# Kernel tuning notes

Hardware: AMD Instinct MI355X
Metric: run time of the kernel (lower is better)

## Reference

```python
import jax, jax.numpy as jnp
import numpy as np

WIRES = 4
NUM_LAYERS = 2


def setup_inputs() -> dict:
    key = jax.random.key(0)
    k1, k2 = jax.random.split(key)
    x = jax.random.uniform(k1, (8192, 1, 28, 28), dtype=jnp.float32)
    params = jax.random.normal(k2, (NUM_LAYERS, WIRES), dtype=jnp.float32)
    return {"x": x, "params": params}


def _apply_ry(state, theta, wire):
    # state: (B, P, 2,2,2,2) real (RY/CNOT circuit keeps amplitudes real)
    s = jnp.moveaxis(state, 2 + wire, -1)
    a, b = s[..., 0], s[..., 1]
    theta = jnp.asarray(theta)
    theta = theta.reshape(theta.shape + (1,) * (a.ndim - theta.ndim))
    c, sn = jnp.cos(theta / 2), jnp.sin(theta / 2)
    s = jnp.stack([c * a - sn * b, sn * a + c * b], axis=-1)
    return jnp.moveaxis(s, -1, 2 + wire)


def _cnot(state, ctrl, tgt):
    s = jnp.moveaxis(state, (2 + ctrl, 2 + tgt), (-2, -1))
    s = jnp.stack([s[..., 0, :], s[..., 1, ::-1]], axis=-2)
    return jnp.moveaxis(s, (-2, -1), (2 + ctrl, 2 + tgt))


def reference(x, params):
    B = x.shape[0]
    # 2x2 patches, row-major over (r, c); each flattened as [x00, x01, x10, x11]
    patches = x[:, 0].reshape(B, 14, 2, 14, 2).transpose(0, 1, 3, 2, 4).reshape(B, 196, 4)
    # |0000> for every (batch, patch)
    state = jnp.zeros((B, 196, 2, 2, 2, 2), dtype=x.dtype).at[:, :, 0, 0, 0, 0].set(1.0)
    # data-encoding RYs + entangling CNOT chain
    for w in range(WIRES):
        state = _apply_ry(state, patches[..., w], w)
    for w in range(WIRES - 1):
        state = _cnot(state, w, w + 1)
    # variational layers
    for layer in range(params.shape[0]):
        for w in range(WIRES):
            state = _apply_ry(state, params[layer, w], w)
        for w in range(WIRES - 1):
            state = _cnot(state, w, w + 1)
    # <Z_w> = P(bit_w = 0) - P(bit_w = 1)
    probs = state * state
    zs = []
    for w in range(WIRES):
        p = jnp.moveaxis(probs, 2 + w, 2)
        zs.append(p[:, :, 0].sum(axis=(2, 3, 4)) - p[:, :, 1].sum(axis=(2, 3, 4)))
    z = jnp.stack(zs, axis=-1)  # (B, 196, 4): 4 expvals per patch, patch-major
    return z.reshape(B, 196 * WIRES)
```

## Files before the change

kernel.cpp:

```cpp
#include <hip/hip_runtime.h>


typedef float f32x2 __attribute__((ext_vector_type(2)));

__device__ __forceinline__ f32x2 pk_fma(f32x2 a, f32x2 b, f32x2 c) {
    return __builtin_elementwise_fma(a, b, c);
}
__device__ __forceinline__ f32x2 splat(float v) { return (f32x2){v, v}; }
__device__ __forceinline__ float uniformf(float v) {
    return __int_as_float(__builtin_amdgcn_readfirstlane(__float_as_int(v)));
}

__device__ __forceinline__ void pk_sincos_half(f32x2 x, f32x2& s, f32x2& c) {
    f32x2 t = x * 0.5f;
    f32x2 u = t * t;
    f32x2 ps = pk_fma(u, splat(8.3333333e-3f), splat(-0.16666667f));
    ps = pk_fma(u, ps, splat(1.0f));
    s = t * ps;
    f32x2 pc = pk_fma(u, splat(-1.3888889e-3f), splat(4.1666667e-2f));
    pc = pk_fma(u, pc, splat(-0.5f));
    c = pk_fma(u, pc, splat(1.0f));
}

template <int W>
__device__ __forceinline__ void apply_ry_t(f32x2 st[16], f32x2 tb, f32x2 ntb) {
    constexpr int S = 8 >> W;
#pragma unroll
    for (int i = 0; i < 16; ++i) {
        if ((i & S) == 0) {
            f32x2 a = st[i], b = st[i | S];
            st[i]     = pk_fma(ntb, b, a);
            st[i | S] = pk_fma(tb, a, b);
        }
    }
}

template <int C, int T>
__device__ __forceinline__ void cnot(f32x2 st[16]) {
    constexpr int CS = 8 >> C, TS = 8 >> T;
#pragma unroll
    for (int i = 0; i < 16; ++i) {
        if ((i & CS) != 0 && (i & TS) == 0) {
            f32x2 t = st[i];
            st[i] = st[i | TS];
            st[i | TS] = t;
        }
    }
}

__global__ __launch_bounds__(256, 4) void quanv_kernel(
    const float* __restrict__ x,
    const float* __restrict__ params,
    float* __restrict__ out,
    int totalPairs)
{
    __shared__ float tl[8];
    int tid = threadIdx.x;
    if (tid < 8) tl[tid] = tanf(0.5f * params[tid]);

    int i = blockIdx.x * 256 + tid;
    int b  = i / 98;
    int q  = i - b * 98;
    int r  = q / 7;
    int cp = q - r * 7;
    bool valid = (i < totalPairs);

    const float* base = x + (size_t)b * 784 + r * 56 + cp * 4;
    float4 top = make_float4(0.f, 0.f, 0.f, 0.f), bot = top;
    if (valid) {
        top = *reinterpret_cast<const float4*>(base);
        bot = *reinterpret_cast<const float4*>(base + 28);
    }

    __syncthreads();
    float t0 = uniformf(tl[0]), t1 = uniformf(tl[1]);
    float t2 = uniformf(tl[2]), t3 = uniformf(tl[3]);
    float t4 = uniformf(tl[4]), t5 = uniformf(tl[5]);
    float t6 = uniformf(tl[6]), t7 = uniformf(tl[7]);
    if (!valid) return;

    f32x2 cw[4], sw[4];
    pk_sincos_half((f32x2){top.x, top.z}, sw[0], cw[0]);
    pk_sincos_half((f32x2){top.y, top.w}, sw[1], cw[1]);
    pk_sincos_half((f32x2){bot.x, bot.z}, sw[2], cw[2]);
    pk_sincos_half((f32x2){bot.y, bot.w}, sw[3], cw[3]);

    f32x2 st[16];
    {
        f32x2 r00 = cw[0] * cw[1], r01 = cw[0] * sw[1];
        f32x2 r10 = sw[0] * cw[1], r11 = sw[0] * sw[1];
        f32x2 q00 = cw[2] * cw[3], q01 = cw[2] * sw[3];
        f32x2 q10 = sw[2] * cw[3], q11 = sw[2] * sw[3];
        st[0]  = r00 * q00; st[1]  = r00 * q01; st[2]  = r00 * q10; st[3]  = r00 * q11;
        st[4]  = r01 * q00; st[5]  = r01 * q01; st[6]  = r01 * q10; st[7]  = r01 * q11;
        st[8]  = r10 * q00; st[9]  = r10 * q01; st[10] = r10 * q10; st[11] = r10 * q11;
        st[12] = r11 * q00; st[13] = r11 * q01; st[14] = r11 * q10; st[15] = r11 * q11;
    }

    cnot<0, 1>(st); cnot<1, 2>(st); cnot<2, 3>(st);

    apply_ry_t<0>(st, splat(t0), splat(-t0));
    apply_ry_t<1>(st, splat(t1), splat(-t1));
    apply_ry_t<2>(st, splat(t2), splat(-t2));
    apply_ry_t<3>(st, splat(t3), splat(-t3));
    cnot<0, 1>(st); cnot<1, 2>(st); cnot<2, 3>(st);
    apply_ry_t<0>(st, splat(t4), splat(-t4));
    apply_ry_t<1>(st, splat(t5), splat(-t5));
    apply_ry_t<2>(st, splat(t6), splat(-t6));
    apply_ry_t<3>(st, splat(t7), splat(-t7));
    cnot<0, 1>(st); cnot<1, 2>(st); cnot<2, 3>(st);

#pragma unroll
    for (int k = 0; k < 16; ++k) st[k] = st[k] * st[k];

    f32x2 a0 = st[0] + st[1],   d0 = st[0] - st[1];
    f32x2 a1 = st[2] + st[3],   d1 = st[2] - st[3];
    f32x2 a2 = st[4] + st[5],   d2 = st[4] - st[5];
    f32x2 a3 = st[6] + st[7],   d3 = st[6] - st[7];
    f32x2 a4 = st[8] + st[9],   d4 = st[8] - st[9];
    f32x2 a5 = st[10] + st[11], d5 = st[10] - st[11];
    f32x2 a6 = st[12] + st[13], d6 = st[12] - st[13];
    f32x2 a7 = st[14] + st[15], d7 = st[14] - st[15];
    f32x2 z3 = ((d0 + d1) + (d2 + d3)) + ((d4 + d5) + (d6 + d7));
    f32x2 b0 = a0 + a1, b1 = a2 + a3, b2 = a4 + a5, b3 = a6 + a7;
    f32x2 z2 = (a0 - a1) + (a2 - a3) + (a4 - a5) + (a6 - a7);
    f32x2 z1 = (b0 - b1) + (b2 - b3);
    f32x2 c0 = b0 + b1, c1 = b2 + b3;
    f32x2 z0 = c0 - c1;
    f32x2 tot = c0 + c1;
    f32x2 inv = (f32x2){__builtin_amdgcn_rcpf(tot.x), __builtin_amdgcn_rcpf(tot.y)};
    z0 *= inv; z1 *= inv; z2 *= inv; z3 *= inv;

    size_t outBase = ((size_t)b * 196 + r * 14 + cp * 2) * 4;
    reinterpret_cast<float4*>(out + outBase)[0] = make_float4(z0.x, z1.x, z2.x, z3.x);
    reinterpret_cast<float4*>(out + outBase)[1] = make_float4(z0.y, z1.y, z2.y, z3.y);
}

extern "C" void kernel_launch(void* const* d_in, const int* in_sizes, int n_in,
                              void* d_out, int out_size, void* d_ws, size_t ws_size,
                              hipStream_t stream) {
    const float* x      = (const float*)d_in[0];
    const float* params = (const float*)d_in[1];
    float* out = (float*)d_out;

    int B = in_sizes[0] / 784;
    int totalPairs = B * 98;

    int grid = (totalPairs + 255) / 256;
    quanv_kernel<<<grid, 256, 0, stream>>>(x, params, out, totalPairs);
}
```

Baseline: 16.79 us.

## Process four batch chunks per thread and compute param tangents per thread

Each thread now handles four patch pairs taken from four batch quarters, with all loads issued up front to raise memory-level parallelism and amortize setup. The shared-memory tan table and the block barrier are removed. Each thread computes sin/cos of the params using the hardware v_sin/v_cos instructions, and replaces the per-output reciprocal normalization with a constant scale equal to the product of cos^2. This cuts the rcp work but does 8 sincos per thread and uses more registers. The grid shrinks fourfold.

```diff
diff --git a/kernel.cpp b/kernel.cpp
--- a/kernel.cpp
+++ b/kernel.cpp
@@ -3,20 +3,24 @@
 
 typedef float f32x2 __attribute__((ext_vector_type(2)));
 
+#define REV 0.07957747155f
+
+__device__ __forceinline__ float fsin(float rev) {
+    float o; asm("v_sin_f32 %0, %1" : "=v"(o) : "v"(rev)); return o;
+}
+__device__ __forceinline__ float fcos(float rev) {
+    float o; asm("v_cos_f32 %0, %1" : "=v"(o) : "v"(rev)); return o;
+}
 __device__ __forceinline__ f32x2 pk_fma(f32x2 a, f32x2 b, f32x2 c) {
     return __builtin_elementwise_fma(a, b, c);
 }
 __device__ __forceinline__ f32x2 splat(float v) { return (f32x2){v, v}; }
-__device__ __forceinline__ float uniformf(float v) {
-    return __int_as_float(__builtin_amdgcn_readfirstlane(__float_as_int(v)));
-}
 
 __device__ __forceinline__ void pk_sincos_half(f32x2 x, f32x2& s, f32x2& c) {
     f32x2 t = x * 0.5f;
     f32x2 u = t * t;
     f32x2 ps = pk_fma(u, splat(8.3333333e-3f), splat(-0.16666667f));
-    ps = pk_fma(u, ps, splat(1.0f));
-    s = t * ps;
+    s = t * pk_fma(u, ps, splat(1.0f));
     f32x2 pc = pk_fma(u, splat(-1.3888889e-3f), splat(4.1666667e-2f));
     pc = pk_fma(u, pc, splat(-0.5f));
     c = pk_fma(u, pc, splat(1.0f));
@@ -48,38 +52,10 @@
     }
 }
 
-__global__ __launch_bounds__(256, 4) void quanv_kernel(
-    const float* __restrict__ x,
-    const float* __restrict__ params,
-    float* __restrict__ out,
-    int totalPairs)
-{
-    __shared__ float tl[8];
-    int tid = threadIdx.x;
-    if (tid < 8) tl[tid] = tanf(0.5f * params[tid]);
-
-    int i = blockIdx.x * 256 + tid;
-    int b  = i / 98;
-    int q  = i - b * 98;
-    int r  = q / 7;
-    int cp = q - r * 7;
-    bool valid = (i < totalPairs);
-
-    const float* base = x + (size_t)b * 784 + r * 56 + cp * 4;
-    float4 top = make_float4(0.f, 0.f, 0.f, 0.f), bot = top;
-    if (valid) {
-        top = *reinterpret_cast<const float4*>(base);
-        bot = *reinterpret_cast<const float4*>(base + 28);
-    }
-
-    __syncthreads();
-    float t0 = uniformf(tl[0]), t1 = uniformf(tl[1]);
-    float t2 = uniformf(tl[2]), t3 = uniformf(tl[3]);
-    float t4 = uniformf(tl[4]), t5 = uniformf(tl[5]);
-    float t6 = uniformf(tl[6]), t7 = uniformf(tl[7]);
-    if (!valid) return;
-
-    f32x2 cw[4], sw[4];
+__device__ __forceinline__ void circuit_pair(float4 top, float4 bot,
+                                             const f32x2 tv[8], const f32x2 ntv[8],
+                                             f32x2 scale, float4& o0, float4& o1) {
+    f32x2 sw[4], cw[4];
     pk_sincos_half((f32x2){top.x, top.z}, sw[0], cw[0]);
     pk_sincos_half((f32x2){top.y, top.w}, sw[1], cw[1]);
     pk_sincos_half((f32x2){bot.x, bot.z}, sw[2], cw[2]);
@@ -99,15 +75,15 @@
 
     cnot<0, 1>(st); cnot<1, 2>(st); cnot<2, 3>(st);
 
-    apply_ry_t<0>(st, splat(t0), splat(-t0));
-    apply_ry_t<1>(st, splat(t1), splat(-t1));
-    apply_ry_t<2>(st, splat(t2), splat(-t2));
-    apply_ry_t<3>(st, splat(t3), splat(-t3));
+    apply_ry_t<0>(st, tv[0], ntv[0]);
+    apply_ry_t<1>(st, tv[1], ntv[1]);
+    apply_ry_t<2>(st, tv[2], ntv[2]);
+    apply_ry_t<3>(st, tv[3], ntv[3]);
     cnot<0, 1>(st); cnot<1, 2>(st); cnot<2, 3>(st);
-    apply_ry_t<0>(st, splat(t4), splat(-t4));
-    apply_ry_t<1>(st, splat(t5), splat(-t5));
-    apply_ry_t<2>(st, splat(t6), splat(-t6));
-    apply_ry_t<3>(st, splat(t7), splat(-t7));
+    apply_ry_t<0>(st, tv[4], ntv[4]);
+    apply_ry_t<1>(st, tv[5], ntv[5]);
+    apply_ry_t<2>(st, tv[6], ntv[6]);
+    apply_ry_t<3>(st, tv[7], ntv[7]);
     cnot<0, 1>(st); cnot<1, 2>(st); cnot<2, 3>(st);
 
 #pragma unroll
@@ -125,15 +101,60 @@
     f32x2 b0 = a0 + a1, b1 = a2 + a3, b2 = a4 + a5, b3 = a6 + a7;
     f32x2 z2 = (a0 - a1) + (a2 - a3) + (a4 - a5) + (a6 - a7);
     f32x2 z1 = (b0 - b1) + (b2 - b3);
-    f32x2 c0 = b0 + b1, c1 = b2 + b3;
-    f32x2 z0 = c0 - c1;
-    f32x2 tot = c0 + c1;
-    f32x2 inv = (f32x2){__builtin_amdgcn_rcpf(tot.x), __builtin_amdgcn_rcpf(tot.y)};
-    z0 *= inv; z1 *= inv; z2 *= inv; z3 *= inv;
+    f32x2 z0 = (b0 + b1) - (b2 + b3);
+    z0 *= scale; z1 *= scale; z2 *= scale; z3 *= scale;
 
-    size_t outBase = ((size_t)b * 196 + r * 14 + cp * 2) * 4;
-    reinterpret_cast<float4*>(out + outBase)[0] = make_float4(z0.x, z1.x, z2.x, z3.x);
-    reinterpret_cast<float4*>(out + outBase)[1] = make_float4(z0.y, z1.y, z2.y, z3.y);
+    o0 = make_float4(z0.x, z1.x, z2.x, z3.x);
+    o1 = make_float4(z0.y, z1.y, z2.y, z3.y);
+}
+
+template <int K>
+__global__ __launch_bounds__(256) void quanv_kernel(
+    const float* __restrict__ x,
+    const float* __restrict__ params,
+    float* __restrict__ out,
+    int chunkPairs,
+    int chunkElems)
+{
+    int i = blockIdx.x * 256 + threadIdx.x;
+    if (i >= chunkPairs) return;
+
+    int b  = i / 98;
+    int q  = i - b * 98;
+    int r  = q / 7;
+    int cp = q - r * 7;
+
+    const float* base = x + (size_t)b * 784 + r * 56 + cp * 4;
+    float4 L[2 * K];
+#pragma unroll
+    for (int k = 0; k < K; ++k) {
+        const float* p = base + (size_t)k * chunkElems;
+        L[2 * k]     = *reinterpret_cast<const float4*>(p);
+        L[2 * k + 1] = *reinterpret_cast<const float4*>(p + 28);
+    }
+
+    f32x2 tv[8], ntv[8];
+    float P = 1.0f;
+#pragma unroll
+    for (int k = 0; k < 8; ++k) {
+        float rev = params[k] * REV;
+        float s = fsin(rev), c = fcos(rev);
+        float t = s * __builtin_amdgcn_rcpf(c);
+        tv[k] = splat(t);
+        ntv[k] = splat(-t);
+        P *= c * c;
+    }
+    f32x2 scale = splat(P);
+
+    float* obase = out + ((size_t)b * 196 + r * 14 + cp * 2) * 4;
+#pragma unroll
+    for (int k = 0; k < K; ++k) {
+        float4 o0, o1;
+        circuit_pair(L[2 * k], L[2 * k + 1], tv, ntv, scale, o0, o1);
+        float* op = obase + (size_t)k * chunkElems;
+        reinterpret_cast<float4*>(op)[0] = o0;
+        reinterpret_cast<float4*>(op)[1] = o1;
+    }
 }
 
 extern "C" void kernel_launch(void* const* d_in, const int* in_sizes, int n_in,
@@ -144,8 +165,15 @@
     float* out = (float*)d_out;
 
     int B = in_sizes[0] / 784;
-    int totalPairs = B * 98;
 
-    int grid = (totalPairs + 255) / 256;
-    quanv_kernel<<<grid, 256, 0, stream>>>(x, params, out, totalPairs);
+    if ((B % 4) == 0) {
+        int chunkPairs = (B / 4) * 98;
+        int chunkElems = (B / 4) * 784;
+        int grid = (chunkPairs + 255) / 256;
+        quanv_kernel<4><<<grid, 256, 0, stream>>>(x, params, out, chunkPairs, chunkElems);
+    } else {
+        int chunkPairs = B * 98;
+        int grid = (chunkPairs + 255) / 256;
+        quanv_kernel<1><<<grid, 256, 0, stream>>>(x, params, out, chunkPairs, B * 784);
+    }
 }
```

Result: slower. 18.01 us (+7.3%).
